# Kernel optimization log

Hardware: AMD Instinct MI355X
Metric: run time of the kernel (lower is better)

Reference implementation:

```python
import jax, jax.numpy as jnp
import numpy as np

B, NPC = 8, 8192          # clouds, points per cloud
RATIO, R = 0.25, 0.2      # fps ratio, radius
C_IN = 64


def _fps_single(pts, s):
    """Farthest point sampling on one cloud. pts: [n,3] -> [s] int32 indices."""
    n = pts.shape[0]

    def step(carry, _):
        mind, last = carry
        dist = jnp.sum((pts - pts[last]) ** 2, axis=-1)   # [n]
        mind = jnp.minimum(mind, dist)
        nxt = jnp.argmax(mind).astype(jnp.int32)
        return (mind, nxt), last

    init = (jnp.full((n,), jnp.inf, pts.dtype), jnp.int32(0))
    (_, _), idx = jax.lax.scan(step, init, None, length=s)
    return idx


def setup_inputs() -> dict:
    key = jax.random.key(0)
    ks = jax.random.split(key, 8)
    N = B * NPC
    x = jax.random.normal(ks[0], (N, C_IN), jnp.float32)
    pos = jax.random.uniform(ks[1], (N, 3), jnp.float32)        # points in unit cube
    batch = jnp.repeat(jnp.arange(B, dtype=jnp.int32), NPC)     # sorted cloud ids, equal sizes
    d = C_IN + 3
    W1 = jax.random.normal(ks[2], (d, 64), jnp.float32) / np.sqrt(d)
    b1 = jnp.zeros((64,), jnp.float32)
    W2 = jax.random.normal(ks[3], (64, 64), jnp.float32) / np.sqrt(64.0)
    b2 = jnp.zeros((64,), jnp.float32)
    W3 = jax.random.normal(ks[4], (64, 128), jnp.float32) / np.sqrt(64.0)
    b3 = jnp.zeros((128,), jnp.float32)
    return {"x": x, "pos": pos, "batch": batch, "num_samples": 32,
            "W1": W1, "b1": b1, "W2": W2, "b2": b2, "W3": W3, "b3": b3}


def reference(x, pos, batch, num_samples, W1, b1, W2, b2, W3, b3):
    K = int(num_samples)
    S = int(NPC * RATIO)
    posb = pos.reshape(B, NPC, 3)
    xb = x.reshape(B, NPC, -1)

    # --- fps(pos, batch, ratio) per cloud ---
    idx = jax.vmap(lambda p: _fps_single(p, S))(posb)           # [B,S]
    q = jax.vmap(lambda p, i: p[i])(posb, idx)                  # [B,S,3] sampled centers

    # --- radius(pos, pos[idx], r, max_num_neighbors=K): K nearest within ball ---
    d2 = jnp.sum((q[:, :, None, :] - posb[:, None, :, :]) ** 2, axis=-1)  # [B,S,NPC]
    neg = jnp.where(d2 <= R * R, -d2, -jnp.inf)
    vals, nidx = jax.lax.top_k(neg, K)                          # [B,S,K]
    valid = vals > -jnp.inf                                     # [B,S,K] (center itself always valid)

    # --- PointConv: h_ij = MLP(concat(x_j, pos_j - pos_i)), max-aggregate over j ---
    x_j = jax.vmap(lambda xc, ic: xc[ic])(xb, nidx)             # [B,S,K,C]
    p_j = jax.vmap(lambda pc, ic: pc[ic])(posb, nidx)           # [B,S,K,3]
    feat = jnp.concatenate([x_j, p_j - q[:, :, None, :]], axis=-1)  # [B,S,K,C+3]
    h = jax.nn.relu(feat @ W1 + b1)
    h = jax.nn.relu(h @ W2 + b2)
    h = h @ W3 + b3                                             # [B,S,K,128]
    h = jnp.where(valid[..., None], h, -jnp.inf)
    out = jnp.max(h, axis=2)                                    # [B,S,128]

    x_out = out.reshape(B * S, -1)
    pos_out = q.reshape(B * S, 3)
    batch_out = jnp.repeat(jnp.arange(B, dtype=jnp.int32), S)
    return x_out, pos_out, batch_out
```

## Files before the change

### kernel.cpp

```cpp
#include <hip/hip_runtime.h>

typedef unsigned long long u64;
typedef unsigned int u32;
typedef float v2f __attribute__((ext_vector_type(2)));

#define NB   8
#define NPC  8192
#define SS   2048
#define KK   32
#define CIN  64
#define NQ   (NB*SS)
#define POS_OUT_OFF   (NQ*128)
#define BATCH_OUT_OFF (NQ*128 + NQ*3)
#define INF64 0x7ff0000000000000ULL

__device__ __forceinline__ v2f pk_add(v2f a, v2f b) {
    v2f r; asm("v_pk_add_f32 %0, %1, %2" : "=v"(r) : "v"(a), "v"(b)); return r;
}
__device__ __forceinline__ v2f pk_mul(v2f a, v2f b) {
    v2f r; asm("v_pk_mul_f32 %0, %1, %2" : "=v"(r) : "v"(a), "v"(b)); return r;
}
__device__ __forceinline__ double mkkey(float m, u32 ni) {
    return __hiloint2double((int)__float_as_uint(m), (int)ni);
}
__device__ __forceinline__ double dpp_wave_max_key(double v) {
#define DPP_LVL(ctrl) { \
    int lo = __double2loint(v), hi = __double2hiint(v); \
    int tlo = __builtin_amdgcn_update_dpp(lo, lo, ctrl, 0xf, 0xf, false); \
    int thi = __builtin_amdgcn_update_dpp(hi, hi, ctrl, 0xf, 0xf, false); \
    v = fmax(v, __hiloint2double(thi, tlo)); }
    DPP_LVL(0x111) DPP_LVL(0x112) DPP_LVL(0x114) DPP_LVL(0x118)
    DPP_LVL(0x142) DPP_LVL(0x143)
#undef DPP_LVL
    return v;
}

__global__ __launch_bounds__(256) void fps_kernel(const float* __restrict__ pos,
                                                  float* __restrict__ out)
{
    __shared__ float lp[NPC*3];
    __shared__ double red[2][4];
    __shared__ unsigned short hist[SS];
    const int tid  = threadIdx.x;
    const int wid  = tid >> 6;
    const int lane = tid & 63;
    const int cloud = blockIdx.x;
    const float* cp = pos + (size_t)cloud * (NPC*3);

    {
        const float4* s4 = (const float4*)cp;
        float4* d4 = (float4*)lp;
        #pragma unroll
        for (int i = 0; i < 24; ++i) d4[tid + i*256] = s4[tid + i*256];
    }
    __syncthreads();

    v2f px[16], py[16], pz[16], mind[16];
    u32 inv[32];
    const float finf = __int_as_float(0x7f800000);
    #pragma unroll
    for (int k = 0; k < 16; ++k) {
        int j = tid*32 + 2*k;
        px[k] = (v2f){lp[j*3+0], lp[j*3+3]};
        py[k] = (v2f){lp[j*3+1], lp[j*3+4]};
        pz[k] = (v2f){lp[j*3+2], lp[j*3+5]};
        mind[k] = (v2f){finf, finf};
    }
    #pragma unroll
    for (int k = 0; k < 32; ++k) inv[k] = ~(u32)(tid*32 + k);

    float cx = lp[0], cy = lp[1], cz = lp[2];
    u32 widx = 0;

    for (int s = 0; s < SS; ++s) {
        if (tid == 0) hist[s] = (unsigned short)widx;
        v2f ncx = (v2f){-cx,-cx}, ncy = (v2f){-cy,-cy}, ncz = (v2f){-cz,-cz};
        double kd[8];
        #pragma unroll
        for (int k = 0; k < 16; ++k) {
            v2f dx = pk_add(px[k], ncx);
            v2f dy = pk_add(py[k], ncy);
            v2f dz = pk_add(pz[k], ncz);
            v2f d  = pk_add(pk_add(pk_mul(dx,dx), pk_mul(dy,dy)), pk_mul(dz,dz));
            float m0 = fminf(mind[k].x, d.x);
            float m1 = fminf(mind[k].y, d.y);
            mind[k].x = m0; mind[k].y = m1;
            double ab = fmax(mkkey(m0, inv[2*k]), mkkey(m1, inv[2*k+1]));
            kd[k & 7] = (k < 8) ? ab : fmax(kd[k & 7], ab);
        }
        #pragma unroll
        for (int st = 4; st >= 1; st >>= 1) {
            #pragma unroll
            for (int k = 0; k < st; ++k) kd[k] = fmax(kd[k], kd[k+st]);
        }
        double wk = dpp_wave_max_key(kd[0]);
        if (lane == 63) red[s&1][wid] = wk;
        __syncthreads();
        const double* rb = red[s&1];
        double g = fmax(fmax(rb[0], rb[1]), fmax(rb[2], rb[3]));
        widx = ~(u32)__double2loint(g);
        cx = lp[widx*3+0]; cy = lp[widx*3+1]; cz = lp[widx*3+2];
    }
    __syncthreads();

    float* qout = out + POS_OUT_OFF   + (size_t)cloud * SS * 3;
    float* bout = out + BATCH_OUT_OFF + (size_t)cloud * SS;
    for (int s = tid; s < SS; s += 256) {
        u32 w = hist[s];
        qout[s*3+0] = lp[w*3+0];
        qout[s*3+1] = lp[w*3+1];
        qout[s*3+2] = lp[w*3+2];
        bout[s] = (float)cloud;
    }
}

#define CAND_MAX 640
__global__ __launch_bounds__(256) void radius_kernel(const float* __restrict__ pos,
                                                     const float* __restrict__ out,
                                                     int* __restrict__ nidx,
                                                     int* __restrict__ ncnt)
{
    __shared__ u64 cand[4][CAND_MAX];
    const int tid  = threadIdx.x;
    const int wid  = tid >> 6;
    const int lane = tid & 63;
    const float R2 = (float)(0.2 * 0.2);
    const float* qpos = out + POS_OUT_OFF;
    u64* cw = cand[wid];

    for (int qq = 0; qq < 4; ++qq) {
        const int q     = blockIdx.x*16 + wid*4 + qq;
        const int cloud = q >> 11;
        const float* cp = pos + (size_t)cloud * (NPC*3);
        float qx = qpos[q*3+0], qy = qpos[q*3+1], qz = qpos[q*3+2];

        int m = 0;
        for (int c = 0; c < NPC/64; ++c) {
            int j = c*64 + lane;
            float dx = __fsub_rn(cp[j*3+0], qx);
            float dy = __fsub_rn(cp[j*3+1], qy);
            float dz = __fsub_rn(cp[j*3+2], qz);
            float d2 = __fadd_rn(__fadd_rn(__fmul_rn(dx,dx), __fmul_rn(dy,dy)), __fmul_rn(dz,dz));
            bool in = (d2 <= R2);
            u64 mk = __ballot(in);
            if (in) {
                int p = m + __popcll(mk & ((1ull << lane) - 1ull));
                if (p < CAND_MAX) cw[p] = ((u64)__float_as_uint(d2) << 32) | (u32)j;
            }
            m += __popcll(mk);
        }
        if (m > CAND_MAX) m = CAND_MAX;

        double kk[10];
        #pragma unroll
        for (int t = 0; t < 10; ++t) {
            int p = t*64 + lane;
            kk[t] = (p < m) ? __longlong_as_double((long long)cw[p])
                            : __longlong_as_double((long long)INF64);
        }
        int cq = (m < KK) ? m : KK;
        int* nq = nidx + (size_t)q * KK;
        int j0 = 0;
        #pragma unroll 1
        for (int r = 0; r < KK; ++r) {
            double lmin = kk[0];
            #pragma unroll
            for (int t = 1; t < 10; ++t) lmin = fmin(lmin, kk[t]);
            #pragma unroll
            for (int off = 32; off >= 1; off >>= 1)
                lmin = fmin(lmin, __shfl_xor(lmin, off));
            u64 lb = (u64)__double_as_longlong(lmin);
            int j = (int)(u32)lb;
            if (r == 0) j0 = j;
            if (lane == 0) nq[r] = (lb == INF64) ? j0 : j;
            #pragma unroll
            for (int t = 0; t < 10; ++t)
                if ((u64)__double_as_longlong(kk[t]) == lb)
                    kk[t] = __longlong_as_double((long long)INF64);
        }
        if (lane == 0) ncnt[q] = cq;
    }
}

__global__ __launch_bounds__(256) void mlp_kernel(const float* __restrict__ x,
                                                  const float* __restrict__ pos,
                                                  const float* __restrict__ W1, const float* __restrict__ b1,
                                                  const float* __restrict__ W2, const float* __restrict__ b2,
                                                  const float* __restrict__ W3, const float* __restrict__ b3,
                                                  const int* __restrict__ nidx, const int* __restrict__ ncnt,
                                                  float* __restrict__ out)
{
    __shared__ float flds[256*69];

    const int tid   = threadIdx.x;
    const int q     = blockIdx.x * 8 + (tid >> 5);
    const int slot  = tid & 31;
    const int cloud = q >> 11;
    const int j     = nidx[q*KK + slot];
    const bool valid = slot < ncnt[q];
    const size_t row = (size_t)cloud * NPC + (size_t)j;

    const float* qp = out + POS_OUT_OFF + (size_t)q*3;
    float qx = qp[0], qy = qp[1], qz = qp[2];

    float* myf = &flds[tid*69];
    {
        const float4* xr = (const float4*)(x + row*CIN);
        #pragma unroll
        for (int i = 0; i < 16; ++i) {
            float4 v = xr[i];
            myf[i*4+0]=v.x; myf[i*4+1]=v.y; myf[i*4+2]=v.z; myf[i*4+3]=v.w;
        }
        myf[64] = __fsub_rn(pos[row*3+0], qx);
        myf[65] = __fsub_rn(pos[row*3+1], qy);
        myf[66] = __fsub_rn(pos[row*3+2], qz);
    }

    float acc[64];
    #pragma unroll
    for (int o = 0; o < 64; ++o) acc[o] = b1[o];
    #pragma unroll 2
    for (int i = 0; i < 67; ++i) {
        float f = myf[i];
        const float4* wr = (const float4*)(W1 + i*64);
        #pragma unroll
        for (int o4 = 0; o4 < 16; ++o4) {
            float4 wv = wr[o4];
            acc[o4*4+0] = fmaf(f, wv.x, acc[o4*4+0]);
            acc[o4*4+1] = fmaf(f, wv.y, acc[o4*4+1]);
            acc[o4*4+2] = fmaf(f, wv.z, acc[o4*4+2]);
            acc[o4*4+3] = fmaf(f, wv.w, acc[o4*4+3]);
        }
    }
    #pragma unroll
    for (int o = 0; o < 64; ++o) myf[o] = fmaxf(acc[o], 0.0f);

    #pragma unroll
    for (int o = 0; o < 64; ++o) acc[o] = b2[o];
    #pragma unroll 2
    for (int i = 0; i < 64; ++i) {
        float f = myf[i];
        const float4* wr = (const float4*)(W2 + i*64);
        #pragma unroll
        for (int o4 = 0; o4 < 16; ++o4) {
            float4 wv = wr[o4];
            acc[o4*4+0] = fmaf(f, wv.x, acc[o4*4+0]);
            acc[o4*4+1] = fmaf(f, wv.y, acc[o4*4+1]);
            acc[o4*4+2] = fmaf(f, wv.z, acc[o4*4+2]);
            acc[o4*4+3] = fmaf(f, wv.w, acc[o4*4+3]);
        }
    }
    #pragma unroll
    for (int o = 0; o < 64; ++o) myf[o] = fmaxf(acc[o], 0.0f);

    float* orow = out + (size_t)q*128;
    const float NEGINF = __int_as_float(0xff800000);
    for (int h = 0; h < 2; ++h) {
        #pragma unroll
        for (int o = 0; o < 64; ++o) acc[o] = b3[h*64 + o];
        const float* w3h = W3 + h*64;
        #pragma unroll 2
        for (int i = 0; i < 64; ++i) {
            float f = myf[i];
            const float4* wr = (const float4*)(w3h + i*128);
            #pragma unroll
            for (int o4 = 0; o4 < 16; ++o4) {
                float4 wv = wr[o4];
                acc[o4*4+0] = fmaf(f, wv.x, acc[o4*4+0]);
                acc[o4*4+1] = fmaf(f, wv.y, acc[o4*4+1]);
                acc[o4*4+2] = fmaf(f, wv.z, acc[o4*4+2]);
                acc[o4*4+3] = fmaf(f, wv.w, acc[o4*4+3]);
            }
        }
        #pragma unroll
        for (int o = 0; o < 64; ++o) if (!valid) acc[o] = NEGINF;
        #pragma unroll
        for (int off = 16; off >= 1; off >>= 1) {
            #pragma unroll
            for (int o = 0; o < 64; ++o) acc[o] = fmaxf(acc[o], __shfl_xor(acc[o], off));
        }
        if (slot == 0) {
            #pragma unroll
            for (int o = 0; o < 64; o += 4) {
                float4 v = make_float4(acc[o], acc[o+1], acc[o+2], acc[o+3]);
                *(float4*)&orow[h*64+o] = v;
            }
        }
    }
}

extern "C" void kernel_launch(void* const* d_in, const int* in_sizes, int n_in,
                              void* d_out, int out_size, void* d_ws, size_t ws_size,
                              hipStream_t stream) {
    const float* x   = (const float*)d_in[0];
    const float* pos = (const float*)d_in[1];
    const float* W1 = (const float*)d_in[4];
    const float* b1 = (const float*)d_in[5];
    const float* W2 = (const float*)d_in[6];
    const float* b2 = (const float*)d_in[7];
    const float* W3 = (const float*)d_in[8];
    const float* b3 = (const float*)d_in[9];
    float* out = (float*)d_out;

    int* nidx = (int*)d_ws;
    int* ncnt = nidx + (size_t)NQ*KK;

    hipLaunchKernelGGL(fps_kernel,    dim3(NB),      dim3(256), 0, stream, pos, out);
    hipLaunchKernelGGL(radius_kernel, dim3(NQ/16),   dim3(256), 0, stream, pos, out, nidx, ncnt);
    hipLaunchKernelGGL(mlp_kernel,    dim3(NQ/8),    dim3(256), 0, stream,
                       x, pos, W1, b1, W2, b2, W3, b3, nidx, ncnt, out);
}
```

Baseline: 2.104 ms.

## Accelerate FPS with spatial grid cells and per-cell max-key pruning

Replaces the brute-force farthest point sampling, which updated all 8192 min-distances every step, with an 8x8x8 spatial grid. Points are bucketed into cells, and each cell keeps a cached max (min-distance, index) key. Each step only recomputes cells whose bounding-box lower bound is below the cell's current max min-distance, and picks the next point with a wave reduction over the 512 cell keys. Far fewer points are touched per step, but the work now goes through shared memory with irregular per-cell loops, and tie-breaking has to stay exact.

```diff
diff --git a/kernel.cpp b/kernel.cpp
--- a/kernel.cpp
+++ b/kernel.cpp
@@ -2,7 +2,6 @@
 
 typedef unsigned long long u64;
 typedef unsigned int u32;
-typedef float v2f __attribute__((ext_vector_type(2)));
 
 #define NB   8
 #define NPC  8192
@@ -13,17 +12,10 @@
 #define POS_OUT_OFF   (NQ*128)
 #define BATCH_OUT_OFF (NQ*128 + NQ*3)
 #define INF64 0x7ff0000000000000ULL
-
-__device__ __forceinline__ v2f pk_add(v2f a, v2f b) {
-    v2f r; asm("v_pk_add_f32 %0, %1, %2" : "=v"(r) : "v"(a), "v"(b)); return r;
-}
-__device__ __forceinline__ v2f pk_mul(v2f a, v2f b) {
-    v2f r; asm("v_pk_mul_f32 %0, %1, %2" : "=v"(r) : "v"(a), "v"(b)); return r;
-}
-__device__ __forceinline__ double mkkey(float m, u32 ni) {
-    return __hiloint2double((int)__float_as_uint(m), (int)ni);
-}
-__device__ __forceinline__ double dpp_wave_max_key(double v) {
+#define NCELL 512
+
+
+__device__ __forceinline__ double wave64_max(double v) {
 #define DPP_LVL(ctrl) { \
     int lo = __double2loint(v), hi = __double2hiint(v); \
     int tlo = __builtin_amdgcn_update_dpp(lo, lo, ctrl, 0xf, 0xf, false); \
@@ -34,83 +26,153 @@
 #undef DPP_LVL
     return v;
 }
+__device__ __forceinline__ double row16_max(double v) {
+#define DPP_LVL(ctrl) { \
+    int lo = __double2loint(v), hi = __double2hiint(v); \
+    int tlo = __builtin_amdgcn_update_dpp(lo, lo, ctrl, 0xf, 0xf, false); \
+    int thi = __builtin_amdgcn_update_dpp(hi, hi, ctrl, 0xf, 0xf, false); \
+    v = fmax(v, __hiloint2double(thi, tlo)); }
+    DPP_LVL(0x111) DPP_LVL(0x112) DPP_LVL(0x114) DPP_LVL(0x118)
+#undef DPP_LVL
+    return v;
+}
 
 __global__ __launch_bounds__(256) void fps_kernel(const float* __restrict__ pos,
                                                   float* __restrict__ out)
 {
-    __shared__ float lp[NPC*3];
-    __shared__ double red[2][4];
-    __shared__ unsigned short hist[SS];
+    __shared__ double cellKey[NCELL];
+    __shared__ float sx[NPC], sy[NPC], sz[NPC];
+    __shared__ float smind[NPC];
+    __shared__ u32 cs[NCELL];
+    __shared__ u32 cnt_hist[1024];
+    __shared__ unsigned short sid[NPC];
+    __shared__ unsigned short wact[4][128];
+    __shared__ u32 ws0_sh;
+
     const int tid  = threadIdx.x;
     const int wid  = tid >> 6;
     const int lane = tid & 63;
     const int cloud = blockIdx.x;
     const float* cp = pos + (size_t)cloud * (NPC*3);
 
+    u32* cnt = cnt_hist;
+    for (int c = tid; c < NCELL; c += 256) cnt[c] = 0;
+    __syncthreads();
+    for (int i = tid; i < NPC; i += 256) {
+        float x = cp[i*3+0], y = cp[i*3+1], z = cp[i*3+2];
+        int cx = (int)(x*8.0f); cx = cx>7?7:cx;
+        int cy = (int)(y*8.0f); cy = cy>7?7:cy;
+        int cz = (int)(z*8.0f); cz = cz>7?7:cz;
+        atomicAdd(&cnt[(cx<<6)|(cy<<3)|cz], 1u);
+    }
+    __syncthreads();
     {
-        const float4* s4 = (const float4*)cp;
-        float4* d4 = (float4*)lp;
-        #pragma unroll
-        for (int i = 0; i < 24; ++i) d4[tid + i*256] = s4[tid + i*256];
+        int c0 = tid, c1 = tid + 256;
+        cs[c0] = cnt[c0]; cs[c1] = cnt[c1];
+        __syncthreads();
+        for (int off = 1; off < NCELL; off <<= 1) {
+            u32 v0 = cs[c0] + ((c0 >= off) ? cs[c0-off] : 0u);
+            u32 v1 = cs[c1] + ((c1 >= off) ? cs[c1-off] : 0u);
+            __syncthreads();
+            cs[c0] = v0; cs[c1] = v1;
+            __syncthreads();
+        }
+        u32 e0 = cs[c0], s0 = e0 - cnt[c0];
+        u32 e1 = cs[c1], s1 = e1 - cnt[c1];
+        cnt[c0] = s0; cnt[c1] = s1;
+        cellKey[c0] = (e0 > s0) ? __hiloint2double(0x7f800000, 0) : 0.0;
+        cellKey[c1] = (e1 > s1) ? __hiloint2double(0x7f800000, 0) : 0.0;
     }
     __syncthreads();
-
-    v2f px[16], py[16], pz[16], mind[16];
-    u32 inv[32];
-    const float finf = __int_as_float(0x7f800000);
-    #pragma unroll
-    for (int k = 0; k < 16; ++k) {
-        int j = tid*32 + 2*k;
-        px[k] = (v2f){lp[j*3+0], lp[j*3+3]};
-        py[k] = (v2f){lp[j*3+1], lp[j*3+4]};
-        pz[k] = (v2f){lp[j*3+2], lp[j*3+5]};
-        mind[k] = (v2f){finf, finf};
-    }
-    #pragma unroll
-    for (int k = 0; k < 32; ++k) inv[k] = ~(u32)(tid*32 + k);
-
-    float cx = lp[0], cy = lp[1], cz = lp[2];
-    u32 widx = 0;
+    for (int i = tid; i < NPC; i += 256) {
+        float x = cp[i*3+0], y = cp[i*3+1], z = cp[i*3+2];
+        int cx = (int)(x*8.0f); cx = cx>7?7:cx;
+        int cy = (int)(y*8.0f); cy = cy>7?7:cy;
+        int cz = (int)(z*8.0f); cz = cz>7?7:cz;
+        u32 slot = atomicAdd(&cnt[(cx<<6)|(cy<<3)|cz], 1u);
+        sx[slot] = x; sy[slot] = y; sz[slot] = z;
+        sid[slot] = (unsigned short)i;
+        smind[slot] = __int_as_float(0x7f800000);
+        if (i == 0) ws0_sh = slot;
+    }
+    __syncthreads();
+
+    unsigned short* hist = (unsigned short*)cnt_hist;
+    u32 ws = ws0_sh;
+    const int g = lane >> 4, sub = lane & 15;
+    const int cidA = (lane << 2) | wid, cidB = ((lane + 64) << 2) | wid;
+    const float bxA = (float)((cidA>>6)&7)*0.125f - 1e-6f;
+    const float byA = (float)((cidA>>3)&7)*0.125f - 1e-6f;
+    const float bzA = (float)( cidA     &7)*0.125f - 1e-6f;
+    const float bxB = (float)((cidB>>6)&7)*0.125f - 1e-6f;
+    const float byB = (float)((cidB>>3)&7)*0.125f - 1e-6f;
+    const float bzB = (float)( cidB     &7)*0.125f - 1e-6f;
+    const float CW = 0.125f + 2e-6f;
 
     for (int s = 0; s < SS; ++s) {
-        if (tid == 0) hist[s] = (unsigned short)widx;
-        v2f ncx = (v2f){-cx,-cx}, ncy = (v2f){-cy,-cy}, ncz = (v2f){-cz,-cz};
-        double kd[8];
-        #pragma unroll
-        for (int k = 0; k < 16; ++k) {
-            v2f dx = pk_add(px[k], ncx);
-            v2f dy = pk_add(py[k], ncy);
-            v2f dz = pk_add(pz[k], ncz);
-            v2f d  = pk_add(pk_add(pk_mul(dx,dx), pk_mul(dy,dy)), pk_mul(dz,dz));
-            float m0 = fminf(mind[k].x, d.x);
-            float m1 = fminf(mind[k].y, d.y);
-            mind[k].x = m0; mind[k].y = m1;
-            double ab = fmax(mkkey(m0, inv[2*k]), mkkey(m1, inv[2*k+1]));
-            kd[k & 7] = (k < 8) ? ab : fmax(kd[k & 7], ab);
-        }
-        #pragma unroll
-        for (int st = 4; st >= 1; st >>= 1) {
-            #pragma unroll
-            for (int k = 0; k < st; ++k) kd[k] = fmax(kd[k], kd[k+st]);
-        }
-        double wk = dpp_wave_max_key(kd[0]);
-        if (lane == 63) red[s&1][wid] = wk;
+        if (s > 0) {
+            double k0 = fmax(cellKey[lane      ], cellKey[lane + 64 ]);
+            double k1 = fmax(cellKey[lane + 128], cellKey[lane + 192]);
+            double k2 = fmax(cellKey[lane + 256], cellKey[lane + 320]);
+            double k3 = fmax(cellKey[lane + 384], cellKey[lane + 448]);
+            double k  = fmax(fmax(k0, k1), fmax(k2, k3));
+            k = wave64_max(k);
+            u32 lo = (u32)__builtin_amdgcn_readlane(__double2loint(k), 63);
+            ws = lo & 8191u;
+        }
+        if (tid == 0) hist[s] = (unsigned short)ws;
+        float ccx = sx[ws], ccy = sy[ws], ccz = sz[ws];
         __syncthreads();
-        const double* rb = red[s&1];
-        double g = fmax(fmax(rb[0], rb[1]), fmax(rb[2], rb[3]));
-        widx = ~(u32)__double2loint(g);
-        cx = lp[widx*3+0]; cy = lp[widx*3+1]; cz = lp[widx*3+2];
-    }
-    __syncthreads();
+
+        float dxA = fmaxf(fmaxf(bxA - ccx, ccx - (bxA + CW)), 0.0f);
+        float dyA = fmaxf(fmaxf(byA - ccy, ccy - (byA + CW)), 0.0f);
+        float dzA = fmaxf(fmaxf(bzA - ccz, ccz - (bzA + CW)), 0.0f);
+        float lbA = dxA*dxA + dyA*dyA + dzA*dzA;
+        float cmA = __uint_as_float(((const u32*)&cellKey[cidA])[1]);
+        bool aA = (lbA * 0.999996f) < cmA;
+        float dxB = fmaxf(fmaxf(bxB - ccx, ccx - (bxB + CW)), 0.0f);
+        float dyB = fmaxf(fmaxf(byB - ccy, ccy - (byB + CW)), 0.0f);
+        float dzB = fmaxf(fmaxf(bzB - ccz, ccz - (bzB + CW)), 0.0f);
+        float lbB = dxB*dxB + dyB*dyB + dzB*dzB;
+        float cmB = __uint_as_float(((const u32*)&cellKey[cidB])[1]);
+        bool aB = (lbB * 0.999996f) < cmB;
+        u64 mA = __ballot(aA);
+        u64 mB = __ballot(aB);
+        u32 nA = (u32)__popcll(mA);
+        if (aA) wact[wid][__popcll(mA & ((1ull<<lane)-1ull))]      = (unsigned short)cidA;
+        if (aB) wact[wid][nA + __popcll(mB & ((1ull<<lane)-1ull))] = (unsigned short)cidB;
+        u32 na = nA + (u32)__popcll(mB);
+
+        for (u32 ai = (u32)g; ai < na; ai += 4) {
+            int cid = wact[wid][ai];
+            u32 st = (cid > 0) ? cs[cid-1] : 0u;
+            u32 en = cs[cid];
+            double fk = 0.0;
+            for (u32 p = st + (u32)sub; p < en; p += 16) {
+                float dx = __fsub_rn(sx[p], ccx);
+                float dy = __fsub_rn(sy[p], ccy);
+                float dz = __fsub_rn(sz[p], ccz);
+                float d2 = __fadd_rn(__fadd_rn(__fmul_rn(dx,dx), __fmul_rn(dy,dy)),
+                                     __fmul_rn(dz,dz));
+                float m = fminf(smind[p], d2);
+                smind[p] = m;
+                u32 lowb = ((8191u - (u32)sid[p]) << 13) | p;
+                fk = fmax(fk, __hiloint2double((int)__float_as_uint(m), (int)lowb));
+            }
+            fk = row16_max(fk);
+            if (sub == 15) cellKey[cid] = fk;
+        }
+        __syncthreads();
+    }
 
     float* qout = out + POS_OUT_OFF   + (size_t)cloud * SS * 3;
     float* bout = out + BATCH_OUT_OFF + (size_t)cloud * SS;
-    for (int s = tid; s < SS; s += 256) {
-        u32 w = hist[s];
-        qout[s*3+0] = lp[w*3+0];
-        qout[s*3+1] = lp[w*3+1];
-        qout[s*3+2] = lp[w*3+2];
-        bout[s] = (float)cloud;
+    for (int s2 = tid; s2 < SS; s2 += 256) {
+        u32 w = hist[s2];
+        qout[s2*3+0] = sx[w];
+        qout[s2*3+1] = sy[w];
+        qout[s2*3+2] = sz[w];
+        bout[s2] = (float)cloud;
     }
 }
 
```

Result: slower. 2.776 ms (+31.9%).

## Pack two clouds per FPS block and read positions directly from global memory

Applied to the files above, without the earlier changes.

The farthest-point-sampling kernel now runs two clouds in one 512-thread block (256 threads per cloud), which halves the grid to four blocks. It also drops the shared-memory copy of each cloud's positions: the per-thread point registers and the selected center are read from global memory, and the per-step reduction buffers and history are indexed per cloud. The aim is to remove the LDS staging and its barrier. In exchange, every one of the 2048 serial steps now waits on a global (cache) load for the next center, and each block-wide barrier couples two independent clouds across eight waves.

```diff
diff --git a/kernel.cpp b/kernel.cpp
--- a/kernel.cpp
+++ b/kernel.cpp
@@ -2,6 +2,7 @@
 
 typedef unsigned long long u64;
 typedef unsigned int u32;
+typedef unsigned short u16;
 typedef float v2f __attribute__((ext_vector_type(2)));
 
 #define NB   8
@@ -35,45 +36,38 @@
     return v;
 }
 
-__global__ __launch_bounds__(256) void fps_kernel(const float* __restrict__ pos,
+__global__ __launch_bounds__(512) void fps_kernel(const float* __restrict__ pos,
                                                   float* __restrict__ out)
 {
-    __shared__ float lp[NPC*3];
-    __shared__ double red[2][4];
-    __shared__ unsigned short hist[SS];
+    __shared__ double red[2][2][4];
+    __shared__ u16 hist[2][SS];
     const int tid  = threadIdx.x;
-    const int wid  = tid >> 6;
+    const int grp  = tid >> 8;
+    const int g    = tid & 255;
+    const int wg   = (tid >> 6) & 3;
     const int lane = tid & 63;
-    const int cloud = blockIdx.x;
+    const int cloud = blockIdx.x * 2 + grp;
     const float* cp = pos + (size_t)cloud * (NPC*3);
-
-    {
-        const float4* s4 = (const float4*)cp;
-        float4* d4 = (float4*)lp;
-        #pragma unroll
-        for (int i = 0; i < 24; ++i) d4[tid + i*256] = s4[tid + i*256];
-    }
-    __syncthreads();
 
     v2f px[16], py[16], pz[16], mind[16];
     u32 inv[32];
     const float finf = __int_as_float(0x7f800000);
     #pragma unroll
     for (int k = 0; k < 16; ++k) {
-        int j = tid*32 + 2*k;
-        px[k] = (v2f){lp[j*3+0], lp[j*3+3]};
-        py[k] = (v2f){lp[j*3+1], lp[j*3+4]};
-        pz[k] = (v2f){lp[j*3+2], lp[j*3+5]};
+        int j = g*32 + 2*k;
+        px[k] = (v2f){cp[j*3+0], cp[j*3+3]};
+        py[k] = (v2f){cp[j*3+1], cp[j*3+4]};
+        pz[k] = (v2f){cp[j*3+2], cp[j*3+5]};
         mind[k] = (v2f){finf, finf};
     }
     #pragma unroll
-    for (int k = 0; k < 32; ++k) inv[k] = ~(u32)(tid*32 + k);
-
-    float cx = lp[0], cy = lp[1], cz = lp[2];
+    for (int k = 0; k < 32; ++k) inv[k] = ~(u32)(g*32 + k);
+
+    float cx = cp[0], cy = cp[1], cz = cp[2];
     u32 widx = 0;
 
     for (int s = 0; s < SS; ++s) {
-        if (tid == 0) hist[s] = (unsigned short)widx;
+        if (g == 0) hist[grp][s] = (u16)widx;
         v2f ncx = (v2f){-cx,-cx}, ncy = (v2f){-cy,-cy}, ncz = (v2f){-cz,-cz};
         double kd[8];
         #pragma unroll
@@ -94,23 +88,23 @@
             for (int k = 0; k < st; ++k) kd[k] = fmax(kd[k], kd[k+st]);
         }
         double wk = dpp_wave_max_key(kd[0]);
-        if (lane == 63) red[s&1][wid] = wk;
+        if (lane == 63) red[grp][s&1][wg] = wk;
         __syncthreads();
-        const double* rb = red[s&1];
-        double g = fmax(fmax(rb[0], rb[1]), fmax(rb[2], rb[3]));
-        widx = ~(u32)__double2loint(g);
-        cx = lp[widx*3+0]; cy = lp[widx*3+1]; cz = lp[widx*3+2];
+        const double* rb = red[grp][s&1];
+        double gk = fmax(fmax(rb[0], rb[1]), fmax(rb[2], rb[3]));
+        widx = ~(u32)__double2loint(gk);
+        cx = cp[widx*3+0]; cy = cp[widx*3+1]; cz = cp[widx*3+2];
     }
     __syncthreads();
 
     float* qout = out + POS_OUT_OFF   + (size_t)cloud * SS * 3;
     float* bout = out + BATCH_OUT_OFF + (size_t)cloud * SS;
-    for (int s = tid; s < SS; s += 256) {
-        u32 w = hist[s];
-        qout[s*3+0] = lp[w*3+0];
-        qout[s*3+1] = lp[w*3+1];
-        qout[s*3+2] = lp[w*3+2];
-        bout[s] = (float)cloud;
+    for (int s2 = g; s2 < SS; s2 += 256) {
+        u32 w = hist[grp][s2];
+        qout[s2*3+0] = cp[w*3+0];
+        qout[s2*3+1] = cp[w*3+1];
+        qout[s2*3+2] = cp[w*3+2];
+        bout[s2] = (float)cloud;
     }
 }
 
@@ -305,7 +299,7 @@
     int* nidx = (int*)d_ws;
     int* ncnt = nidx + (size_t)NQ*KK;
 
-    hipLaunchKernelGGL(fps_kernel,    dim3(NB),      dim3(256), 0, stream, pos, out);
+    hipLaunchKernelGGL(fps_kernel,    dim3(NB/2),    dim3(512), 0, stream, pos, out);
     hipLaunchKernelGGL(radius_kernel, dim3(NQ/16),   dim3(256), 0, stream, pos, out, nidx, ncnt);
     hipLaunchKernelGGL(mlp_kernel,    dim3(NQ/8),    dim3(256), 0, stream,
                        x, pos, W1, b1, W2, b2, W3, b3, nidx, ncnt, out);
```

Result: slower. 3.396 ms (+61.4%).
